# Kernel optimization log

Hardware: AMD Instinct MI355X
Metric: run time of the kernel (lower is better)

The kernel has to match this reference:

```python
import jax, jax.numpy as jnp
import numpy as np
from math import sqrt

B, S, Q, L = 16, 1024, 8, 512
D_FEA, D_KEYS, D_MODEL = 128, 128, 128


def setup_inputs() -> dict:
    key = jax.random.key(0)
    ks = jax.random.split(key, 10)
    s = 0.02
    return {
        "target_embedding": jax.random.normal(ks[0], (B, S, D_FEA), dtype=jnp.float32),
        "source_embedding": jax.random.normal(ks[1], (B, Q, L, D_KEYS), dtype=jnp.float32),
        "Wq": jax.random.normal(ks[2], (D_FEA, D_MODEL), dtype=jnp.float32) * s,
        "bq": jnp.zeros((D_MODEL,), dtype=jnp.float32),
        "Wk": jax.random.normal(ks[3], (D_KEYS, D_MODEL), dtype=jnp.float32) * s,
        "bk": jnp.zeros((D_MODEL,), dtype=jnp.float32),
        "Wv": jax.random.normal(ks[4], (D_KEYS, D_MODEL), dtype=jnp.float32) * s,
        "bv": jnp.zeros((D_MODEL,), dtype=jnp.float32),
        "Wo": jax.random.normal(ks[5], (D_MODEL, D_FEA), dtype=jnp.float32) * s,
        "bo": jnp.zeros((D_FEA,), dtype=jnp.float32),
    }


def reference(target_embedding, source_embedding, Wq, bq, Wk, bk, Wv, bv, Wo, bo):
    # Projections
    q = target_embedding @ Wq + bq            # [B,S,E]
    k = source_embedding @ Wk + bk            # [B,Q,L,E]
    v = source_embedding @ Wv + bv            # [B,Q,L,E]
    E = q.shape[-1]
    scale = 1.0 / sqrt(E)
    # Nonstandard 4D scores: [B,Q,S,L]
    scores = jnp.einsum('bse,bqle->bqsl', q, k)
    A = jax.nn.softmax(scale * scores, axis=-1)  # softmax over l; dropout = identity (eval)
    # Weighted sum reduces over BOTH q and l -> [B,S,E]
    out = jnp.einsum('bqsl,bqle->bse', A, v)
    return out @ Wo + bo
```

## Files before the change

kernel.cpp:

```cpp
#include <hip/hip_runtime.h>
#include <hip/hip_bf16.h>

#define TB 16
#define TS 1024
#define TQ 8
#define TL 512
#define TD 128

typedef __attribute__((ext_vector_type(8))) short bf16x8;
typedef __attribute__((ext_vector_type(4))) short short4v;
typedef __attribute__((ext_vector_type(4))) float f32x4;
typedef __attribute__((ext_vector_type(4))) float float4v;

__device__ __forceinline__ short f2bf(float f) {
    union { float fv; unsigned u; } v; v.fv = f;
    unsigned r = v.u + 0x7fffu + ((v.u >> 16) & 1u);
    return (short)(r >> 16);
}

#define OFF_Q   0u
#define OFF_K   (4u << 20)
#define OFF_V   (OFF_K + (16u << 20))
#define OFF_ATT (OFF_V + (16u << 20))
#define OFF_W   (OFF_ATT + (4u << 20))

__global__ void prep_w(const float* __restrict__ Wq, const float* __restrict__ Wk,
                       const float* __restrict__ Wv, const float* __restrict__ Wo,
                       short* __restrict__ wt) {
    const float* srcs[4] = {Wq, Wk, Wv, Wo};
    const float* s = srcs[blockIdx.x];
    short* dst = wt + blockIdx.x * (TD * TD);
    for (int i = threadIdx.x; i < TD * TD; i += blockDim.x) {
        int k = i >> 7, e = i & 127;
        dst[e * TD + k] = f2bf(s[i]);
    }
}

__global__ __launch_bounds__(256) void proj_rm(const float* __restrict__ X,
                                               const short* __restrict__ Wt,
                                               const float* __restrict__ bias,
                                               short* __restrict__ Y) {
    __shared__ short xt[32][136];
    const int t = threadIdx.x;
    const int lane = t & 63, w = t >> 6;
    const int lane16 = lane & 15, g = lane >> 4;
    const int r0 = blockIdx.x * 32;

#pragma unroll
    for (int it = 0; it < 4; ++it) {
        int f4 = t + it * 256;
        int row = f4 >> 5, col = (f4 & 31) * 4;
        float4v x = *reinterpret_cast<const float4v*>(&X[(long)(r0 + row) * TD + col]);
        short4v s;
        s[0] = f2bf(x[0]); s[1] = f2bf(x[1]); s[2] = f2bf(x[2]); s[3] = f2bf(x[3]);
        *reinterpret_cast<short4v*>(&xt[row][col]) = s;
    }
    __syncthreads();

    const int n0 = w * 32;
    bf16x8 a[2][4];
#pragma unroll
    for (int mi = 0; mi < 2; ++mi)
#pragma unroll
        for (int kt = 0; kt < 4; ++kt)
            a[mi][kt] = *reinterpret_cast<const bf16x8*>(&xt[mi * 16 + lane16][kt * 32 + g * 8]);

    const f32x4 Z = {0.f, 0.f, 0.f, 0.f};
    f32x4 acc[2][2] = {{Z, Z}, {Z, Z}};
#pragma unroll
    for (int ni = 0; ni < 2; ++ni)
#pragma unroll
        for (int kt = 0; kt < 4; ++kt) {
            bf16x8 b = *reinterpret_cast<const bf16x8*>(
                &Wt[(n0 + ni * 16 + lane16) * TD + kt * 32 + g * 8]);
#pragma unroll
            for (int mi = 0; mi < 2; ++mi)
                acc[mi][ni] = __builtin_amdgcn_mfma_f32_16x16x32_bf16(a[mi][kt], b, acc[mi][ni], 0, 0, 0);
        }

#pragma unroll
    for (int mi = 0; mi < 2; ++mi)
#pragma unroll
        for (int ni = 0; ni < 2; ++ni) {
            int e = n0 + ni * 16 + lane16;
            float bb = bias[e];
#pragma unroll
            for (int reg = 0; reg < 4; ++reg) {
                int row = r0 + mi * 16 + g * 4 + reg;
                Y[(long)row * TD + e] = f2bf(acc[mi][ni][reg] + bb);
            }
        }
}

__global__ __launch_bounds__(256) void proj_kv(const float* __restrict__ X,
                                               const short* __restrict__ Wtk,
                                               const float* __restrict__ biask,
                                               const short* __restrict__ Wtv,
                                               const float* __restrict__ biasv,
                                               short* __restrict__ K,
                                               short* __restrict__ Vf) {
    __shared__ short xt[32][136];
    const int t = threadIdx.x;
    const int lane = t & 63, w = t >> 6;
    const int lane16 = lane & 15, g = lane >> 4;
    const int r0 = blockIdx.x * 32;

#pragma unroll
    for (int it = 0; it < 4; ++it) {
        int f4 = t + it * 256;
        int row = f4 >> 5, col = (f4 & 31) * 4;
        float4v x = *reinterpret_cast<const float4v*>(&X[(long)(r0 + row) * TD + col]);
        short4v s;
        s[0] = f2bf(x[0]); s[1] = f2bf(x[1]); s[2] = f2bf(x[2]); s[3] = f2bf(x[3]);
        *reinterpret_cast<short4v*>(&xt[row][col]) = s;
    }
    __syncthreads();

    const int n0 = w * 32;
    bf16x8 a[2][4];
#pragma unroll
    for (int mi = 0; mi < 2; ++mi)
#pragma unroll
        for (int kt = 0; kt < 4; ++kt)
            a[mi][kt] = *reinterpret_cast<const bf16x8*>(&xt[mi * 16 + lane16][kt * 32 + g * 8]);

    const f32x4 Z = {0.f, 0.f, 0.f, 0.f};
    f32x4 ak[2][2] = {{Z, Z}, {Z, Z}};
    f32x4 av[2][2] = {{Z, Z}, {Z, Z}};
#pragma unroll
    for (int ni = 0; ni < 2; ++ni)
#pragma unroll
        for (int kt = 0; kt < 4; ++kt) {
            bf16x8 bk = *reinterpret_cast<const bf16x8*>(
                &Wtk[(n0 + ni * 16 + lane16) * TD + kt * 32 + g * 8]);
            bf16x8 bv = *reinterpret_cast<const bf16x8*>(
                &Wtv[(n0 + ni * 16 + lane16) * TD + kt * 32 + g * 8]);
#pragma unroll
            for (int mi = 0; mi < 2; ++mi) {
                ak[mi][ni] = __builtin_amdgcn_mfma_f32_16x16x32_bf16(a[mi][kt], bk, ak[mi][ni], 0, 0, 0);
                av[mi][ni] = __builtin_amdgcn_mfma_f32_16x16x32_bf16(a[mi][kt], bv, av[mi][ni], 0, 0, 0);
            }
        }

#pragma unroll
    for (int mi = 0; mi < 2; ++mi)
#pragma unroll
        for (int ni = 0; ni < 2; ++ni) {
            int e = n0 + ni * 16 + lane16;
            float bbk = biask[e], bbv = biasv[e];
#pragma unroll
            for (int reg = 0; reg < 4; ++reg) {
                int row = r0 + mi * 16 + g * 4 + reg;
                K[(long)row * TD + e] = f2bf(ak[mi][ni][reg] + bbk);
            }
            int row0 = r0 + mi * 16 + g * 4;
            int bq = row0 >> 9;
            int l = row0 & 511;
            int k32 = l >> 5, j8 = (l >> 3) & 3, jb = l & 7;
            long off = (long)bq * (TL * TD) +
                       ((((long)(k32 * 8 + (e >> 4)) * 4 + j8) * 16) + (e & 15)) * 8 + jb;
            short4v sv;
#pragma unroll
            for (int reg = 0; reg < 4; ++reg) sv[reg] = f2bf(av[mi][ni][reg] + bbv);
            *reinterpret_cast<short4v*>(&Vf[off]) = sv;
        }
}

__global__ __launch_bounds__(256, 2) void attn_k(const short* __restrict__ qb,
                                                 const short* __restrict__ kb,
                                                 const short* __restrict__ vf,
                                                 short* __restrict__ attn) {
    __shared__ float cmb[2][4][2][16][2];
    __shared__ float red[2][2][8][4][16][4];
    const int t = threadIdx.x;
    const int lane = t & 63, w = t >> 6;
    const int lane16 = lane & 15, g = lane >> 4;

    int idx = blockIdx.y * gridDim.x + blockIdx.x;
    int xcd = idx & 7, slot = idx >> 3;
    const int b = xcd * 2 + (slot >> 5);
    const int s0 = (slot & 31) * 32;

    bf16x8 qf[2][4];
#pragma unroll
    for (int sg = 0; sg < 2; ++sg) {
        const short* qrow = qb + (long)(b * TS + s0 + sg * 16 + lane16) * TD;
#pragma unroll
        for (int kt = 0; kt < 4; ++kt)
            qf[sg][kt] = *reinterpret_cast<const bf16x8*>(qrow + kt * 32 + g * 8);
    }

    const f32x4 Z = {0.f, 0.f, 0.f, 0.f};
    f32x4 o[2][8];
#pragma unroll
    for (int sg = 0; sg < 2; ++sg)
#pragma unroll
        for (int et = 0; et < 8; ++et) o[sg][et] = Z;

    const float C = 0.08838834764831845f * 1.4426950408889634f;
    const int arow = 8 * (lane16 >> 2) + (lane16 & 3);

    for (int qi = 0; qi < TQ; ++qi) {
        const long kvb = (long)(b * TQ + qi) * (TL * TD);
        const short* Kw = kb + kvb + (long)(w * 128) * TD;

        f32x4 sacc[2][8];
#pragma unroll
        for (int sg = 0; sg < 2; ++sg)
#pragma unroll
            for (int lt = 0; lt < 8; ++lt) sacc[sg][lt] = Z;
#pragma unroll
        for (int lt = 0; lt < 8; ++lt) {
            const short* krow = Kw + (long)(32 * (lt >> 1) + 4 * (lt & 1) + arow) * TD;
            bf16x8 ka[4];
#pragma unroll
            for (int kt = 0; kt < 4; ++kt)
                ka[kt] = *reinterpret_cast<const bf16x8*>(krow + kt * 32 + g * 8);
#pragma unroll
            for (int kt = 0; kt < 4; ++kt) {
                sacc[0][lt] = __builtin_amdgcn_mfma_f32_16x16x32_bf16(ka[kt], qf[0][kt], sacc[0][lt], 0, 0, 0);
                sacc[1][lt] = __builtin_amdgcn_mfma_f32_16x16x32_bf16(ka[kt], qf[1][kt], sacc[1][lt], 0, 0, 0);
            }
        }

        float Fs[2];
#pragma unroll
        for (int sg = 0; sg < 2; ++sg) {
            float mx = sacc[sg][0][0];
#pragma unroll
            for (int lt = 0; lt < 8; ++lt)
#pragma unroll
                for (int r = 0; r < 4; ++r) mx = fmaxf(mx, sacc[sg][lt][r]);
            mx = fmaxf(mx, __shfl_xor(mx, 16));
            mx = fmaxf(mx, __shfl_xor(mx, 32));
            float sum = 0.f;
#pragma unroll
            for (int lt = 0; lt < 8; ++lt)
#pragma unroll
                for (int r = 0; r < 4; ++r) {
                    float e = exp2f((sacc[sg][lt][r] - mx) * C);
                    sacc[sg][lt][r] = e;
                    sum += e;
                }
            sum += __shfl_xor(sum, 16);
            sum += __shfl_xor(sum, 32);
            if (lane < 16) {
                cmb[qi & 1][w][sg][lane16][0] = mx;
                cmb[qi & 1][w][sg][lane16][1] = sum;
            }
            Fs[sg] = mx;
        }
        __syncthreads();
#pragma unroll
        for (int sg = 0; sg < 2; ++sg) {
            float m0 = cmb[qi & 1][0][sg][lane16][0];
            float m1 = cmb[qi & 1][1][sg][lane16][0];
            float m2 = cmb[qi & 1][2][sg][lane16][0];
            float m3 = cmb[qi & 1][3][sg][lane16][0];
            float mg = fmaxf(fmaxf(m0, m1), fmaxf(m2, m3));
            float S = cmb[qi & 1][0][sg][lane16][1] * exp2f((m0 - mg) * C)
                    + cmb[qi & 1][1][sg][lane16][1] * exp2f((m1 - mg) * C)
                    + cmb[qi & 1][2][sg][lane16][1] * exp2f((m2 - mg) * C)
                    + cmb[qi & 1][3][sg][lane16][1] * exp2f((m3 - mg) * C);
            Fs[sg] = exp2f((Fs[sg] - mg) * C) / S;
        }

        bf16x8 pa[2][4];
#pragma unroll
        for (int sg = 0; sg < 2; ++sg)
#pragma unroll
            for (int kt = 0; kt < 4; ++kt) {
#pragma unroll
                for (int j = 0; j < 4; ++j)
                    pa[sg][kt][j] = f2bf(sacc[sg][2 * kt][j] * Fs[sg]);
#pragma unroll
                for (int j = 0; j < 4; ++j)
                    pa[sg][kt][4 + j] = f2bf(sacc[sg][2 * kt + 1][j] * Fs[sg]);
            }

#pragma unroll
        for (int kt = 0; kt < 4; ++kt) {
            const short* vbase = vf + kvb + ((long)(w * 4 + kt) * 4096) + g * 128 + lane16 * 8;
#pragma unroll
            for (int et = 0; et < 8; ++et) {
                bf16x8 vb = *reinterpret_cast<const bf16x8*>(vbase + et * 512);
                o[0][et] = __builtin_amdgcn_mfma_f32_16x16x32_bf16(pa[0][kt], vb, o[0][et], 0, 0, 0);
                o[1][et] = __builtin_amdgcn_mfma_f32_16x16x32_bf16(pa[1][kt], vb, o[1][et], 0, 0, 0);
            }
        }
    }

    if (w >= 2) {
#pragma unroll
        for (int sg = 0; sg < 2; ++sg)
#pragma unroll
            for (int et = 0; et < 8; ++et)
                *reinterpret_cast<f32x4*>(&red[w - 2][sg][et][g][lane16][0]) = o[sg][et];
    }
    __syncthreads();
    if (w < 2) {
#pragma unroll
        for (int sg = 0; sg < 2; ++sg)
#pragma unroll
            for (int et = 0; et < 8; ++et)
                o[sg][et] += *reinterpret_cast<f32x4*>(&red[w][sg][et][g][lane16][0]);
    }
    __syncthreads();
    if (w == 1) {
#pragma unroll
        for (int sg = 0; sg < 2; ++sg)
#pragma unroll
            for (int et = 0; et < 8; ++et)
                *reinterpret_cast<f32x4*>(&red[0][sg][et][g][lane16][0]) = o[sg][et];
    }
    __syncthreads();
    if (w == 0) {
#pragma unroll
        for (int sg = 0; sg < 2; ++sg)
#pragma unroll
            for (int et = 0; et < 8; ++et) {
                o[sg][et] += *reinterpret_cast<f32x4*>(&red[0][sg][et][g][lane16][0]);
#pragma unroll
                for (int reg = 0; reg < 4; ++reg) {
                    int s = s0 + sg * 16 + g * 4 + reg;
                    attn[(long)(b * TS + s) * TD + et * 16 + lane16] = f2bf(o[sg][et][reg]);
                }
            }
    }
}

__global__ __launch_bounds__(256) void final_proj(const short* __restrict__ A,
                                                  const short* __restrict__ Wt,
                                                  const float* __restrict__ bias,
                                                  float* __restrict__ out) {
    const int t = threadIdx.x;
    const int lane = t & 63, w = t >> 6;
    const int lane16 = lane & 15, g = lane >> 4;
    const int r0 = blockIdx.x * 32;
    const int n0 = w * 32;

    bf16x8 a[2][4];
#pragma unroll
    for (int mi = 0; mi < 2; ++mi)
#pragma unroll
        for (int kt = 0; kt < 4; ++kt)
            a[mi][kt] = *reinterpret_cast<const bf16x8*>(
                &A[(long)(r0 + mi * 16 + lane16) * TD + kt * 32 + g * 8]);

    const f32x4 Z = {0.f, 0.f, 0.f, 0.f};
    f32x4 acc[2][2] = {{Z, Z}, {Z, Z}};
#pragma unroll
    for (int ni = 0; ni < 2; ++ni)
#pragma unroll
        for (int kt = 0; kt < 4; ++kt) {
            bf16x8 b = *reinterpret_cast<const bf16x8*>(
                &Wt[(n0 + ni * 16 + lane16) * TD + kt * 32 + g * 8]);
#pragma unroll
            for (int mi = 0; mi < 2; ++mi)
                acc[mi][ni] = __builtin_amdgcn_mfma_f32_16x16x32_bf16(a[mi][kt], b, acc[mi][ni], 0, 0, 0);
        }

#pragma unroll
    for (int mi = 0; mi < 2; ++mi)
#pragma unroll
        for (int ni = 0; ni < 2; ++ni) {
            int e = n0 + ni * 16 + lane16;
            float bb = bias[e];
#pragma unroll
            for (int reg = 0; reg < 4; ++reg) {
                int row = r0 + mi * 16 + g * 4 + reg;
                out[(long)row * TD + e] = acc[mi][ni][reg] + bb;
            }
        }
}

extern "C" void kernel_launch(void* const* d_in, const int* in_sizes, int n_in,
                              void* d_out, int out_size, void* d_ws, size_t ws_size,
                              hipStream_t stream) {
    (void)in_sizes; (void)n_in; (void)out_size; (void)ws_size;
    const float* target = (const float*)d_in[0];
    const float* source = (const float*)d_in[1];
    const float* Wq = (const float*)d_in[2];
    const float* bq = (const float*)d_in[3];
    const float* Wk = (const float*)d_in[4];
    const float* bk = (const float*)d_in[5];
    const float* Wv = (const float*)d_in[6];
    const float* bv = (const float*)d_in[7];
    const float* Wo = (const float*)d_in[8];
    const float* bo = (const float*)d_in[9];

    char* ws = (char*)d_ws;
    short* qb = (short*)(ws + OFF_Q);
    short* kb = (short*)(ws + OFF_K);
    short* vf = (short*)(ws + OFF_V);
    short* at = (short*)(ws + OFF_ATT);
    short* wt = (short*)(ws + OFF_W);
    float* out = (float*)d_out;

    prep_w<<<4, 256, 0, stream>>>(Wq, Wk, Wv, Wo, wt);
    proj_rm<<<(TB * TS) / 32, 256, 0, stream>>>(target, wt + 0 * TD * TD, bq, qb);
    proj_kv<<<(TB * TQ * TL) / 32, 256, 0, stream>>>(source, wt + 1 * TD * TD, bk,
                                                     wt + 2 * TD * TD, bv, kb, vf);
    dim3 g3(TS / 32, TB);
    attn_k<<<g3, 256, 0, stream>>>(qb, kb, vf, at);
    final_proj<<<(TB * TS) / 32, 256, 0, stream>>>(at, wt + 3 * TD * TD, bo, out);
}
```

Before: 237.4 us.

## Split attention over Q halves, fuse Q/K/V projections, combine partials in output projection

The attention kernel now splits the Q loop into two halves per block, doubling the grid to 1024 blocks with occupancy hint raised to 4. One half writes bf16 partials to workspace and the other writes fp32 partials into the output buffer. The final projection sums both partials before the Wo matmul. It also merges the Q and KV projection launches into one kernel, spreads weight prep over 32 blocks, and swaps MFMA operand order so K/Q/output stores are vectorised. The aim is more parallelism and fewer launches, at the cost of extra partial-sum traffic and a bf16 rounding of one partial.

```diff
diff --git a/kernel.cpp b/kernel.cpp
--- a/kernel.cpp
+++ b/kernel.cpp
@@ -17,34 +17,48 @@
     unsigned r = v.u + 0x7fffu + ((v.u >> 16) & 1u);
     return (short)(r >> 16);
 }
+__device__ __forceinline__ float bf2f(short s) {
+    union { unsigned u; float f; } v; v.u = ((unsigned)(unsigned short)s) << 16;
+    return v.f;
+}
 
 #define OFF_Q   0u
 #define OFF_K   (4u << 20)
 #define OFF_V   (OFF_K + (16u << 20))
-#define OFF_ATT (OFF_V + (16u << 20))
-#define OFF_W   (OFF_ATT + (4u << 20))
+#define OFF_P0  (OFF_V + (16u << 20))
+#define OFF_W   (OFF_P0 + (4u << 20))
 
 __global__ void prep_w(const float* __restrict__ Wq, const float* __restrict__ Wk,
                        const float* __restrict__ Wv, const float* __restrict__ Wo,
                        short* __restrict__ wt) {
     const float* srcs[4] = {Wq, Wk, Wv, Wo};
-    const float* s = srcs[blockIdx.x];
-    short* dst = wt + blockIdx.x * (TD * TD);
-    for (int i = threadIdx.x; i < TD * TD; i += blockDim.x) {
-        int k = i >> 7, e = i & 127;
-        dst[e * TD + k] = f2bf(s[i]);
-    }
-}
-
-__global__ __launch_bounds__(256) void proj_rm(const float* __restrict__ X,
-                                               const short* __restrict__ Wt,
-                                               const float* __restrict__ bias,
-                                               short* __restrict__ Y) {
+    const int m = blockIdx.x >> 3;
+    const float* s = srcs[m];
+    short* dst = wt + m * (TD * TD);
+    const int off = (blockIdx.x & 7) * 2048;
+    for (int i = threadIdx.x; i < 2048; i += 256) {
+        int idx = off + i;
+        int k = idx >> 7, e = idx & 127;
+        dst[e * TD + k] = f2bf(s[idx]);
+    }
+}
+
+__global__ __launch_bounds__(256) void proj_all(const float* __restrict__ target,
+                                                const float* __restrict__ source,
+                                                const short* __restrict__ wt,
+                                                const float* __restrict__ biasq,
+                                                const float* __restrict__ biask,
+                                                const float* __restrict__ biasv,
+                                                short* __restrict__ qb,
+                                                short* __restrict__ kb,
+                                                short* __restrict__ vf) {
     __shared__ short xt[32][136];
     const int t = threadIdx.x;
     const int lane = t & 63, w = t >> 6;
     const int lane16 = lane & 15, g = lane >> 4;
-    const int r0 = blockIdx.x * 32;
+    const bool iskv = blockIdx.x < 2048;
+    const int r0 = (iskv ? blockIdx.x : (blockIdx.x - 2048)) * 32;
+    const float* X = iskv ? source : target;
 
 #pragma unroll
     for (int it = 0; it < 4; ++it) {
@@ -66,120 +80,94 @@
             a[mi][kt] = *reinterpret_cast<const bf16x8*>(&xt[mi * 16 + lane16][kt * 32 + g * 8]);
 
     const f32x4 Z = {0.f, 0.f, 0.f, 0.f};
-    f32x4 acc[2][2] = {{Z, Z}, {Z, Z}};
-#pragma unroll
-    for (int ni = 0; ni < 2; ++ni)
-#pragma unroll
-        for (int kt = 0; kt < 4; ++kt) {
-            bf16x8 b = *reinterpret_cast<const bf16x8*>(
-                &Wt[(n0 + ni * 16 + lane16) * TD + kt * 32 + g * 8]);
-#pragma unroll
-            for (int mi = 0; mi < 2; ++mi)
-                acc[mi][ni] = __builtin_amdgcn_mfma_f32_16x16x32_bf16(a[mi][kt], b, acc[mi][ni], 0, 0, 0);
-        }
-
-#pragma unroll
-    for (int mi = 0; mi < 2; ++mi)
-#pragma unroll
-        for (int ni = 0; ni < 2; ++ni) {
-            int e = n0 + ni * 16 + lane16;
-            float bb = bias[e];
-#pragma unroll
-            for (int reg = 0; reg < 4; ++reg) {
-                int row = r0 + mi * 16 + g * 4 + reg;
-                Y[(long)row * TD + e] = f2bf(acc[mi][ni][reg] + bb);
-            }
-        }
-}
-
-__global__ __launch_bounds__(256) void proj_kv(const float* __restrict__ X,
-                                               const short* __restrict__ Wtk,
-                                               const float* __restrict__ biask,
-                                               const short* __restrict__ Wtv,
-                                               const float* __restrict__ biasv,
-                                               short* __restrict__ K,
-                                               short* __restrict__ Vf) {
-    __shared__ short xt[32][136];
-    const int t = threadIdx.x;
-    const int lane = t & 63, w = t >> 6;
-    const int lane16 = lane & 15, g = lane >> 4;
-    const int r0 = blockIdx.x * 32;
-
-#pragma unroll
-    for (int it = 0; it < 4; ++it) {
-        int f4 = t + it * 256;
-        int row = f4 >> 5, col = (f4 & 31) * 4;
-        float4v x = *reinterpret_cast<const float4v*>(&X[(long)(r0 + row) * TD + col]);
-        short4v s;
-        s[0] = f2bf(x[0]); s[1] = f2bf(x[1]); s[2] = f2bf(x[2]); s[3] = f2bf(x[3]);
-        *reinterpret_cast<short4v*>(&xt[row][col]) = s;
-    }
-    __syncthreads();
-
-    const int n0 = w * 32;
-    bf16x8 a[2][4];
-#pragma unroll
-    for (int mi = 0; mi < 2; ++mi)
-#pragma unroll
-        for (int kt = 0; kt < 4; ++kt)
-            a[mi][kt] = *reinterpret_cast<const bf16x8*>(&xt[mi * 16 + lane16][kt * 32 + g * 8]);
-
-    const f32x4 Z = {0.f, 0.f, 0.f, 0.f};
-    f32x4 ak[2][2] = {{Z, Z}, {Z, Z}};
-    f32x4 av[2][2] = {{Z, Z}, {Z, Z}};
-#pragma unroll
-    for (int ni = 0; ni < 2; ++ni)
-#pragma unroll
-        for (int kt = 0; kt < 4; ++kt) {
-            bf16x8 bk = *reinterpret_cast<const bf16x8*>(
-                &Wtk[(n0 + ni * 16 + lane16) * TD + kt * 32 + g * 8]);
-            bf16x8 bv = *reinterpret_cast<const bf16x8*>(
-                &Wtv[(n0 + ni * 16 + lane16) * TD + kt * 32 + g * 8]);
-#pragma unroll
-            for (int mi = 0; mi < 2; ++mi) {
-                ak[mi][ni] = __builtin_amdgcn_mfma_f32_16x16x32_bf16(a[mi][kt], bk, ak[mi][ni], 0, 0, 0);
-                av[mi][ni] = __builtin_amdgcn_mfma_f32_16x16x32_bf16(a[mi][kt], bv, av[mi][ni], 0, 0, 0);
-            }
-        }
-
-#pragma unroll
-    for (int mi = 0; mi < 2; ++mi)
-#pragma unroll
-        for (int ni = 0; ni < 2; ++ni) {
-            int e = n0 + ni * 16 + lane16;
-            float bbk = biask[e], bbv = biasv[e];
-#pragma unroll
-            for (int reg = 0; reg < 4; ++reg) {
-                int row = r0 + mi * 16 + g * 4 + reg;
-                K[(long)row * TD + e] = f2bf(ak[mi][ni][reg] + bbk);
-            }
-            int row0 = r0 + mi * 16 + g * 4;
-            int bq = row0 >> 9;
-            int l = row0 & 511;
-            int k32 = l >> 5, j8 = (l >> 3) & 3, jb = l & 7;
-            long off = (long)bq * (TL * TD) +
-                       ((((long)(k32 * 8 + (e >> 4)) * 4 + j8) * 16) + (e & 15)) * 8 + jb;
-            short4v sv;
-#pragma unroll
-            for (int reg = 0; reg < 4; ++reg) sv[reg] = f2bf(av[mi][ni][reg] + bbv);
-            *reinterpret_cast<short4v*>(&Vf[off]) = sv;
-        }
-}
-
-__global__ __launch_bounds__(256, 2) void attn_k(const short* __restrict__ qb,
+    if (iskv) {
+        const short* Wtk = wt + 1 * TD * TD;
+        const short* Wtv = wt + 2 * TD * TD;
+        f32x4 ak[2][2] = {{Z, Z}, {Z, Z}};
+        f32x4 av[2][2] = {{Z, Z}, {Z, Z}};
+#pragma unroll
+        for (int ni = 0; ni < 2; ++ni)
+#pragma unroll
+            for (int kt = 0; kt < 4; ++kt) {
+                bf16x8 bkf = *reinterpret_cast<const bf16x8*>(
+                    &Wtk[(n0 + ni * 16 + lane16) * TD + kt * 32 + g * 8]);
+                bf16x8 bvf = *reinterpret_cast<const bf16x8*>(
+                    &Wtv[(n0 + ni * 16 + lane16) * TD + kt * 32 + g * 8]);
+#pragma unroll
+                for (int mi = 0; mi < 2; ++mi) {
+                    ak[mi][ni] = __builtin_amdgcn_mfma_f32_16x16x32_bf16(bkf, a[mi][kt], ak[mi][ni], 0, 0, 0);
+                    av[mi][ni] = __builtin_amdgcn_mfma_f32_16x16x32_bf16(a[mi][kt], bvf, av[mi][ni], 0, 0, 0);
+                }
+            }
+#pragma unroll
+        for (int mi = 0; mi < 2; ++mi)
+#pragma unroll
+            for (int ni = 0; ni < 2; ++ni) {
+                int e0 = n0 + ni * 16 + g * 4;
+                float4v kb4 = *reinterpret_cast<const float4v*>(&biask[e0]);
+                int row = r0 + mi * 16 + lane16;
+                short4v ks;
+#pragma unroll
+                for (int reg = 0; reg < 4; ++reg) ks[reg] = f2bf(ak[mi][ni][reg] + kb4[reg]);
+                *reinterpret_cast<short4v*>(&kb[(long)row * TD + e0]) = ks;
+                int e = n0 + ni * 16 + lane16;
+                float bbv = biasv[e];
+                int row0 = r0 + mi * 16 + g * 4;
+                int bq = row0 >> 9;
+                int l = row0 & 511;
+                int k32 = l >> 5, j8 = (l >> 3) & 3, jb = l & 7;
+                long off = (long)bq * (TL * TD) +
+                           ((((long)(k32 * 8 + (e >> 4)) * 4 + j8) * 16) + (e & 15)) * 8 + jb;
+                short4v sv;
+#pragma unroll
+                for (int reg = 0; reg < 4; ++reg) sv[reg] = f2bf(av[mi][ni][reg] + bbv);
+                *reinterpret_cast<short4v*>(&vf[off]) = sv;
+            }
+    } else {
+        const short* Wtq = wt;
+        f32x4 aq[2][2] = {{Z, Z}, {Z, Z}};
+#pragma unroll
+        for (int ni = 0; ni < 2; ++ni)
+#pragma unroll
+            for (int kt = 0; kt < 4; ++kt) {
+                bf16x8 bqf = *reinterpret_cast<const bf16x8*>(
+                    &Wtq[(n0 + ni * 16 + lane16) * TD + kt * 32 + g * 8]);
+#pragma unroll
+                for (int mi = 0; mi < 2; ++mi)
+                    aq[mi][ni] = __builtin_amdgcn_mfma_f32_16x16x32_bf16(bqf, a[mi][kt], aq[mi][ni], 0, 0, 0);
+            }
+#pragma unroll
+        for (int mi = 0; mi < 2; ++mi)
+#pragma unroll
+            for (int ni = 0; ni < 2; ++ni) {
+                int e0 = n0 + ni * 16 + g * 4;
+                float4v qb4 = *reinterpret_cast<const float4v*>(&biasq[e0]);
+                int row = r0 + mi * 16 + lane16;
+                short4v qs;
+#pragma unroll
+                for (int reg = 0; reg < 4; ++reg) qs[reg] = f2bf(aq[mi][ni][reg] + qb4[reg]);
+                *reinterpret_cast<short4v*>(&qb[(long)row * TD + e0]) = qs;
+            }
+    }
+}
+
+__global__ __launch_bounds__(256, 4) void attn_k(const short* __restrict__ qb,
                                                  const short* __restrict__ kb,
                                                  const short* __restrict__ vf,
-                                                 short* __restrict__ attn) {
+                                                 short* __restrict__ po0,
+                                                 float* __restrict__ po1) {
     __shared__ float cmb[2][4][2][16][2];
     __shared__ float red[2][2][8][4][16][4];
     const int t = threadIdx.x;
     const int lane = t & 63, w = t >> 6;
     const int lane16 = lane & 15, g = lane >> 4;
 
-    int idx = blockIdx.y * gridDim.x + blockIdx.x;
+    int idx = blockIdx.x;
     int xcd = idx & 7, slot = idx >> 3;
-    const int b = xcd * 2 + (slot >> 5);
-    const int s0 = (slot & 31) * 32;
+    const int b = xcd * 2 + (slot >> 6);
+    const int rem = slot & 63;
+    const int qh = rem >> 5;
+    const int s0 = (rem & 31) * 32;
 
     bf16x8 qf[2][4];
 #pragma unroll
@@ -200,7 +188,7 @@
     const float C = 0.08838834764831845f * 1.4426950408889634f;
     const int arow = 8 * (lane16 >> 2) + (lane16 & 3);
 
-    for (int qi = 0; qi < TQ; ++qi) {
+    for (int qi = qh * 4; qi < qh * 4 + 4; ++qi) {
         const long kvb = (long)(b * TQ + qi) * (TL * TD);
         const short* Kw = kb + kvb + (long)(w * 128) * TD;
 
@@ -323,16 +311,18 @@
 #pragma unroll
                 for (int reg = 0; reg < 4; ++reg) {
                     int s = s0 + sg * 16 + g * 4 + reg;
-                    attn[(long)(b * TS + s) * TD + et * 16 + lane16] = f2bf(o[sg][et][reg]);
+                    long addr = (long)(b * TS + s) * TD + et * 16 + lane16;
+                    if (qh == 0) po0[addr] = f2bf(o[sg][et][reg]);
+                    else         po1[addr] = o[sg][et][reg];
                 }
             }
     }
 }
 
-__global__ __launch_bounds__(256) void final_proj(const short* __restrict__ A,
-                                                  const short* __restrict__ Wt,
-                                                  const float* __restrict__ bias,
-                                                  float* __restrict__ out) {
+__global__ __launch_bounds__(256) void comb_proj(const short* __restrict__ po0,
+                                                 const short* __restrict__ Wt,
+                                                 const float* __restrict__ bias,
+                                                 float* __restrict__ out) {
     const int t = threadIdx.x;
     const int lane = t & 63, w = t >> 6;
     const int lane16 = lane & 15, g = lane >> 4;
@@ -343,9 +333,19 @@
 #pragma unroll
     for (int mi = 0; mi < 2; ++mi)
 #pragma unroll
-        for (int kt = 0; kt < 4; ++kt)
-            a[mi][kt] = *reinterpret_cast<const bf16x8*>(
-                &A[(long)(r0 + mi * 16 + lane16) * TD + kt * 32 + g * 8]);
+        for (int kt = 0; kt < 4; ++kt) {
+            long base = (long)(r0 + mi * 16 + lane16) * TD + kt * 32 + g * 8;
+            float4v x0 = *reinterpret_cast<const float4v*>(&out[base]);
+            float4v x1 = *reinterpret_cast<const float4v*>(&out[base + 4]);
+            bf16x8 p0 = *reinterpret_cast<const bf16x8*>(&po0[base]);
+            bf16x8 af;
+#pragma unroll
+            for (int j = 0; j < 4; ++j) af[j] = f2bf(x0[j] + bf2f(p0[j]));
+#pragma unroll
+            for (int j = 0; j < 4; ++j) af[4 + j] = f2bf(x1[j] + bf2f(p0[4 + j]));
+            a[mi][kt] = af;
+        }
+    __syncthreads();
 
     const f32x4 Z = {0.f, 0.f, 0.f, 0.f};
     f32x4 acc[2][2] = {{Z, Z}, {Z, Z}};
@@ -353,24 +353,24 @@
     for (int ni = 0; ni < 2; ++ni)
 #pragma unroll
         for (int kt = 0; kt < 4; ++kt) {
-            bf16x8 b = *reinterpret_cast<const bf16x8*>(
+            bf16x8 wf = *reinterpret_cast<const bf16x8*>(
                 &Wt[(n0 + ni * 16 + lane16) * TD + kt * 32 + g * 8]);
 #pragma unroll
             for (int mi = 0; mi < 2; ++mi)
-                acc[mi][ni] = __builtin_amdgcn_mfma_f32_16x16x32_bf16(a[mi][kt], b, acc[mi][ni], 0, 0, 0);
+                acc[mi][ni] = __builtin_amdgcn_mfma_f32_16x16x32_bf16(wf, a[mi][kt], acc[mi][ni], 0, 0, 0);
         }
 
 #pragma unroll
     for (int mi = 0; mi < 2; ++mi)
 #pragma unroll
         for (int ni = 0; ni < 2; ++ni) {
-            int e = n0 + ni * 16 + lane16;
-            float bb = bias[e];
-#pragma unroll
-            for (int reg = 0; reg < 4; ++reg) {
-                int row = r0 + mi * 16 + g * 4 + reg;
-                out[(long)row * TD + e] = acc[mi][ni][reg] + bb;
-            }
+            int e0 = n0 + ni * 16 + g * 4;
+            float4v b4 = *reinterpret_cast<const float4v*>(&bias[e0]);
+            int row = r0 + mi * 16 + lane16;
+            f32x4 res;
+#pragma unroll
+            for (int reg = 0; reg < 4; ++reg) res[reg] = acc[mi][ni][reg] + b4[reg];
+            *reinterpret_cast<f32x4*>(&out[(long)row * TD + e0]) = res;
         }
 }
 
@@ -390,18 +390,15 @@
     const float* bo = (const float*)d_in[9];
 
     char* ws = (char*)d_ws;
-    short* qb = (short*)(ws + OFF_Q);
-    short* kb = (short*)(ws + OFF_K);
-    short* vf = (short*)(ws + OFF_V);
-    short* at = (short*)(ws + OFF_ATT);
-    short* wt = (short*)(ws + OFF_W);
+    short* qb  = (short*)(ws + OFF_Q);
+    short* kb  = (short*)(ws + OFF_K);
+    short* vf  = (short*)(ws + OFF_V);
+    short* po0 = (short*)(ws + OFF_P0);
+    short* wt  = (short*)(ws + OFF_W);
     float* out = (float*)d_out;
 
-    prep_w<<<4, 256, 0, stream>>>(Wq, Wk, Wv, Wo, wt);
-    proj_rm<<<(TB * TS) / 32, 256, 0, stream>>>(target, wt + 0 * TD * TD, bq, qb);
-    proj_kv<<<(TB * TQ * TL) / 32, 256, 0, stream>>>(source, wt + 1 * TD * TD, bk,
-                                                     wt + 2 * TD * TD, bv, kb, vf);
-    dim3 g3(TS / 32, TB);
-    attn_k<<<g3, 256, 0, stream>>>(qb, kb, vf, at);
-    final_proj<<<(TB * TS) / 32, 256, 0, stream>>>(at, wt + 3 * TD * TD, bo, out);
-}
+    prep_w<<<32, 256, 0, stream>>>(Wq, Wk, Wv, Wo, wt);
+    proj_all<<<2560, 256, 0, stream>>>(target, source, wt, bq, bk, bv, qb, kb, vf);
+    attn_k<<<1024, 256, 0, stream>>>(qb, kb, vf, po0, out);
+    comb_proj<<<512, 256, 0, stream>>>(po0, wt + 3 * TD * TD, bo, out);
+}
```

New measurement: 299.1 us. +26.0%, slower.
